# Kernel tuning notes

Measured on AMD Instinct MI355X. Metric: run time of the kernel, lower is better.

The kernel has to match this reference:

```python
import jax, jax.numpy as jnp
import numpy as np

H = 50   # hidden size (hard-coded in module)
O = 10   # fc output size


def _xavier(key, shape):
    # torch nn.init.xavier_normal_: std = sqrt(2 / (fan_in + fan_out)), fan_out=shape[0], fan_in=shape[1]
    std = (2.0 / (shape[0] + shape[1])) ** 0.5
    return jax.random.normal(key, shape, dtype=jnp.float32) * std


def setup_inputs() -> dict:
    key = jax.random.key(0)
    ks = jax.random.split(key, 9)
    B, T = 4096, 512
    x = jax.random.normal(ks[0], (B, T, 1), dtype=jnp.float32)
    z = lambda n: jnp.zeros((n,), dtype=jnp.float32)
    return {
        "x": x,
        "W_ih1": _xavier(ks[1], (H, 1)),  "W_hh1": _xavier(ks[2], (H, H)),
        "b_ih1": z(H), "b_hh1": z(H),
        "W_ih2": _xavier(ks[3], (H, H)),  "W_hh2": _xavier(ks[4], (H, H)),
        "b_ih2": z(H), "b_hh2": z(H),
        "W_ih3": _xavier(ks[5], (H, H)),  "W_hh3": _xavier(ks[6], (H, H)),
        "b_ih3": z(H), "b_hh3": z(H),
        "W_fc": _xavier(ks[7], (O, H)), "b_fc": z(O),
    }


def reference(x, W_ih1, W_hh1, b_ih1, b_hh1,
              W_ih2, W_hh2, b_ih2, b_hh2,
              W_ih3, W_hh3, b_ih3, b_hh3,
              W_fc, b_fc):
    B = x.shape[0]
    h0 = jnp.zeros((B, H), dtype=x.dtype)

    def step(carry, xt):  # xt: [B, 1]
        h1, h2, h3 = carry
        h1 = jnp.tanh(xt @ W_ih1.T + b_ih1 + h1 @ W_hh1.T + b_hh1)
        h2 = jnp.tanh(h1 @ W_ih2.T + b_ih2 + h2 @ W_hh2.T + b_hh2)
        h3 = jnp.tanh(h2 @ W_ih3.T + b_ih3 + h3 @ W_hh3.T + b_hh3)
        return (h1, h2, h3), None

    xs = jnp.swapaxes(x, 0, 1)  # [T, B, 1]
    (h1, h2, h3), _ = jax.lax.scan(step, (h0, h0, h0), xs)
    return h3 @ W_fc.T + b_fc  # [B, 10]
```

## Files before the change

kernel.cpp:

```cpp
#include <hip/hip_runtime.h>

typedef __attribute__((ext_vector_type(8))) short bf16x8;
typedef __attribute__((ext_vector_type(4))) float f32x4;

#define MFMA(a, b, c) __builtin_amdgcn_mfma_f32_16x16x32_bf16((a), (b), (c), 0, 0, 0)

#define TANH_SCALE 2.8853900817779268f

__device__ __forceinline__ short f2bf(float f) {
    union { float f; unsigned u; } v; v.f = f;
    unsigned r = v.u + 0x7fffu + ((v.u >> 16) & 1u);
    return (short)(r >> 16);
}
__device__ __forceinline__ float bf2f(short h) {
    union { unsigned u; float f; } v;
    v.u = ((unsigned)(unsigned short)h) << 16;
    return v.f;
}
__device__ __forceinline__ void wsplit(float w, short& hi, short& lo) {
    hi = f2bf(w);
    lo = f2bf(w - bf2f(hi));
}
__device__ __forceinline__ float tanh_ps(float s) {
    float z = __builtin_amdgcn_exp2f(s);
    return fmaf(-2.0f, __builtin_amdgcn_rcpf(z + 1.0f), 1.0f);
}
__device__ __forceinline__ unsigned cvt_pk_bf16(float a, float b) {
    unsigned r;
    asm("v_cvt_pk_bf16_f32 %0, %1, %2" : "=v"(r) : "v"(a), "v"(b));
    return r;
}

__device__ __forceinline__ void makeA2(const float* __restrict__ W, int jrow, int kbase,
                                       bf16x8& Ahi, bf16x8& Alo) {
#pragma unroll
    for (int i = 0; i < 8; ++i) {
        int m = kbase + i;
        short h = 0, l = 0;
        if (jrow < 50 && m < 50) wsplit(W[jrow * 50 + m] * TANH_SCALE, h, l);
        Ahi[i] = h; Alo[i] = l;
    }
}

__device__ __forceinline__ int swz(int row, int byteInRow) {
    return (row << 8) + (byteInRow ^ ((row & 15) << 4));
}
__device__ __forceinline__ bf16x8 ldsO(const short* hall, int off) {
    return *(const bf16x8*)((const char*)hall + off);
}
__device__ __forceinline__ float ldsR(const short* buf, int row, int col) {
    return bf2f(*(const short*)((const char*)buf + swz(row, col << 1)));
}

__device__ __forceinline__ void storeH(short* hall, int off, float t0, float t1, float t2, float t3) {
    uint2 hv;
    hv.x = cvt_pk_bf16(t0, t1);
    hv.y = cvt_pk_bf16(t2, t3);
    *(uint2*)((char*)hall + off) = hv;
}
__device__ __forceinline__ void storeZ(short* hall, int off) {
    uint2 zz; zz.x = 0u; zz.y = 0u;
    *(uint2*)((char*)hall + off) = zz;
}

template<bool ZOUT>
__device__ __forceinline__ void phaseX(
    short* hall, int layerid,
    int i0o, int i1o, int s0o, int s1o, int woff,
    const float* xrow, int bcol,
    const f32x4& bv, const f32x4& w1f,
    const bf16x8& Ih0, const bf16x8& Ih1,
    const bf16x8& Hh0, const bf16x8& Hh1, const bf16x8& Hl0, const bf16x8& Hl1,
    const f32x4& zc)
{
    if (layerid == 0) {
        float xf = xrow[bcol];
        f32x4 c1i;
        c1i[0] = fmaf(w1f[0], xf, bv[0]);
        c1i[1] = fmaf(w1f[1], xf, bv[1]);
        c1i[2] = fmaf(w1f[2], xf, bv[2]);
        c1i[3] = fmaf(w1f[3], xf, bv[3]);
        bf16x8 s0 = ldsO(hall, s0o), s1 = ldsO(hall, s1o);
        f32x4 c0 = MFMA(Hh0, s0, c1i);
        f32x4 c1 = MFMA(Hh1, s1, zc);
        c0 = MFMA(Hl0, s0, c0);
        c1 = MFMA(Hl1, s1, c1);
        float t0 = tanh_ps(c0[0] + c1[0]);
        float t1 = tanh_ps(c0[1] + c1[1]);
        float t2 = tanh_ps(c0[2] + c1[2]);
        float t3 = tanh_ps(c0[3] + c1[3]);
        storeH(hall, woff, t0, t1, t2, t3);
    } else {
        bf16x8 i0 = ldsO(hall, i0o), i1 = ldsO(hall, i1o);
        bf16x8 s0 = ldsO(hall, s0o), s1 = ldsO(hall, s1o);
        f32x4 c0 = MFMA(Ih0, i0, bv);
        f32x4 c1 = MFMA(Ih1, i1, zc);
        c0 = MFMA(Hh0, s0, c0);
        c1 = MFMA(Hh1, s1, c1);
        c0 = MFMA(Hl0, s0, c0);
        c1 = MFMA(Hl1, s1, c1);
        if (ZOUT) {
            storeZ(hall, woff);
        } else {
            float t0 = tanh_ps(c0[0] + c1[0]);
            float t1 = tanh_ps(c0[1] + c1[1]);
            float t2 = tanh_ps(c0[2] + c1[2]);
            float t3 = tanh_ps(c0[3] + c1[3]);
            storeH(hall, woff, t0, t1, t2, t3);
        }
    }
    __syncthreads();
}

__global__ __launch_bounds__(768, 1)
void rnn3_kernel(const float* __restrict__ x,
                 const float* __restrict__ Wih1, const float* __restrict__ Whh1,
                 const float* __restrict__ bih1, const float* __restrict__ bhh1,
                 const float* __restrict__ Wih2, const float* __restrict__ Whh2,
                 const float* __restrict__ bih2, const float* __restrict__ bhh2,
                 const float* __restrict__ Wih3, const float* __restrict__ Whh3,
                 const float* __restrict__ bih3, const float* __restrict__ bhh3,
                 const float* __restrict__ Wfc,  const float* __restrict__ bfc,
                 float* __restrict__ out)
{
    __shared__ __align__(16) short hall[6][2048];
    __shared__ float xls[514 * 17 + 8];

    const int tid  = threadIdx.x;
    const int lane = tid & 63;
    const int w    = tid >> 6;
    const int stripe  = w & 3;
    const int layerid = w >> 2;
    const int g    = lane >> 4;
    const int l15  = lane & 15;
    const int jrow = (stripe << 4) | l15;
    const int bcol = l15;
    const int jout0 = (stripe << 4) + (g << 2);
    const int b0   = blockIdx.x * 16;

    { int* z = (int*)hall; for (int k = tid; k < 6144; k += 768) z[k] = 0; }

    {
        const float4* xg = (const float4*)(x + (size_t)b0 * 512);
        for (int idx = tid; idx < 2048; idx += 768) {
            float4 v = xg[idx];
            int b = idx >> 7, t0 = (idx & 127) << 2;
            xls[(t0 + 0) * 17 + b] = v.x;
            xls[(t0 + 1) * 17 + b] = v.y;
            xls[(t0 + 2) * 17 + b] = v.z;
            xls[(t0 + 3) * 17 + b] = v.w;
        }
        if (tid < 42) xls[512 * 17 + tid] = 0.0f;
    }

    const float* WI; const float* WH; const float* bi; const float* bh;
    if (layerid == 0)      { WI = Wih1; WH = Whh1; bi = bih1; bh = bhh1; }
    else if (layerid == 1) { WI = Wih2; WH = Whh2; bi = bih2; bh = bhh2; }
    else                   { WI = Wih3; WH = Whh3; bi = bih3; bh = bhh3; }

    bf16x8 zf8 = {0,0,0,0,0,0,0,0};
    bf16x8 Ih0 = zf8, Ih1 = zf8;
    bf16x8 Hh0, Hl0, Hh1, Hl1;
    makeA2(WH, jrow, (g << 3),      Hh0, Hl0);
    makeA2(WH, jrow, 32 + (g << 3), Hh1, Hl1);
    if (layerid != 0) {
        bf16x8 d0, d1;
        makeA2(WI, jrow, (g << 3),      Ih0, d0);
        makeA2(WI, jrow, 32 + (g << 3), Ih1, d1);
    }

    f32x4 bv, w1f;
#pragma unroll
    for (int r = 0; r < 4; ++r) {
        int j = jout0 + r;
        bool v = j < 50;
        bv[r]  = v ? ((bi[j] + bh[j]) * TANH_SCALE) : 0.0f;
        w1f[r] = (layerid == 0 && v) ? (Wih1[j] * TANH_SCALE) : 0.0f;
    }
    const f32x4 zc = {0.f, 0.f, 0.f, 0.f};

    const int o0 = swz(bcol, (0 << 6) + (g << 4));
    const int o1 = swz(bcol, (1 << 6) + (g << 4));
    const int wbyte = swz(bcol, jout0 << 1);
    const int inb = (layerid == 2) ? 1 : 0;
    const int stb = layerid;
    const int A_i0 = (inb * 2 + 1) * 4096 + o0, A_i1 = (inb * 2 + 1) * 4096 + o1;
    const int A_s0 = (stb * 2 + 1) * 4096 + o0, A_s1 = (stb * 2 + 1) * 4096 + o1;
    const int B_i0 = (inb * 2 + 0) * 4096 + o0, B_i1 = (inb * 2 + 0) * 4096 + o1;
    const int B_s0 = (stb * 2 + 0) * 4096 + o0, B_s1 = (stb * 2 + 0) * 4096 + o1;
    const int wofA = (layerid * 2 + 0) * 4096 + wbyte;
    const int wofB = (layerid * 2 + 1) * 4096 + wbyte;

    __syncthreads();

    phaseX<true>(&hall[0][0], layerid, A_i0, A_i1, A_s0, A_s1, wofA,
                 &xls[0], bcol, bv, w1f, Ih0, Ih1, Hh0, Hh1, Hl0, Hl1, zc);
    if (layerid == 2) {
        phaseX<true>(&hall[0][0], layerid, B_i0, B_i1, B_s0, B_s1, wofB,
                     &xls[17], bcol, bv, w1f, Ih0, Ih1, Hh0, Hh1, Hl0, Hl1, zc);
    } else {
        phaseX<false>(&hall[0][0], layerid, B_i0, B_i1, B_s0, B_s1, wofB,
                      &xls[17], bcol, bv, w1f, Ih0, Ih1, Hh0, Hh1, Hl0, Hl1, zc);
    }

    for (int i = 2; i < 512; i += 2) {
        phaseX<false>(&hall[0][0], layerid, A_i0, A_i1, A_s0, A_s1, wofA,
                      &xls[i * 17], bcol, bv, w1f, Ih0, Ih1, Hh0, Hh1, Hl0, Hl1, zc);
        phaseX<false>(&hall[0][0], layerid, B_i0, B_i1, B_s0, B_s1, wofB,
                      &xls[(i + 1) * 17], bcol, bv, w1f, Ih0, Ih1, Hh0, Hh1, Hl0, Hl1, zc);
    }

    phaseX<false>(&hall[0][0], layerid, A_i0, A_i1, A_s0, A_s1, wofA,
                  &xls[512 * 17], bcol, bv, w1f, Ih0, Ih1, Hh0, Hh1, Hl0, Hl1, zc);
    phaseX<false>(&hall[0][0], layerid, B_i0, B_i1, B_s0, B_s1, wofB,
                  &xls[513 * 17], bcol, bv, w1f, Ih0, Ih1, Hh0, Hh1, Hl0, Hl1, zc);

    if (w < 4) {
        const short* h3f = &hall[5][0];
        int o = (w << 2) | g;
        int b = bcol;
        if (o < 10) {
            float acc = bfc[o];
            for (int k = 0; k < 50; ++k)
                acc += ldsR(h3f, b, k) * Wfc[o * 50 + k];
            out[(size_t)(b0 + b) * 10 + o] = acc;
        }
    }
}

extern "C" void kernel_launch(void* const* d_in, const int* in_sizes, int n_in,
                              void* d_out, int out_size, void* d_ws, size_t ws_size,
                              hipStream_t stream) {
    const float* x    = (const float*)d_in[0];
    const float* Wih1 = (const float*)d_in[1];
    const float* Whh1 = (const float*)d_in[2];
    const float* bih1 = (const float*)d_in[3];
    const float* bhh1 = (const float*)d_in[4];
    const float* Wih2 = (const float*)d_in[5];
    const float* Whh2 = (const float*)d_in[6];
    const float* bih2 = (const float*)d_in[7];
    const float* bhh2 = (const float*)d_in[8];
    const float* Wih3 = (const float*)d_in[9];
    const float* Whh3 = (const float*)d_in[10];
    const float* bih3 = (const float*)d_in[11];
    const float* bhh3 = (const float*)d_in[12];
    const float* Wfc  = (const float*)d_in[13];
    const float* bfc  = (const float*)d_in[14];
    float* out = (float*)d_out;

    dim3 grid(256), block(768);
    hipLaunchKernelGGL(rnn3_kernel, grid, block, 0, stream,
                       x, Wih1, Whh1, bih1, bhh1,
                       Wih2, Whh2, bih2, bhh2,
                       Wih3, Whh3, bih3, bhh3,
                       Wfc, bfc, out);
}
```

Baseline: 185.2 us.

## Merge layers 2 and 3 into one wave group, cut block to 512 threads

Restructures the wavefront-to-layer mapping so that 4 waves handle layer 1 and 4 waves compute both layers 2 and 3 together, with interleaved MFMA chains. The block shrinks from 768 to 512 threads, so fewer waves take part in each per-step barrier. The aim is to balance work, since layer 1 has fewer MFMAs, and to overlap the two independent MFMA chains inside one wave. The trade-off is that the merged waves hold twice as many weight registers and do twice the MFMA and tanh work per step, which lengthens the critical path per phase.

```diff
diff --git a/kernel.cpp b/kernel.cpp
--- a/kernel.cpp
+++ b/kernel.cpp
@@ -63,56 +63,76 @@
     *(uint2*)((char*)hall + off) = zz;
 }
 
-template<bool ZOUT>
-__device__ __forceinline__ void phaseX(
-    short* hall, int layerid,
-    int i0o, int i1o, int s0o, int s1o, int woff,
+template<bool Z2, bool Z3>
+__device__ __forceinline__ void phaseY(
+    short* hall, bool isL1,
+    int r1a, int r1b, int r2a, int r2b, int r3a, int r3b,
+    int wo1, int wo2, int wo3,
     const float* xrow, int bcol,
-    const f32x4& bv, const f32x4& w1f,
-    const bf16x8& Ih0, const bf16x8& Ih1,
-    const bf16x8& Hh0, const bf16x8& Hh1, const bf16x8& Hl0, const bf16x8& Hl1,
+    const f32x4& b1v, const f32x4& w1f,
+    const bf16x8& A1h0, const bf16x8& A1h1, const bf16x8& A1l0, const bf16x8& A1l1,
+    const f32x4& bv2, const bf16x8& I2h0, const bf16x8& I2h1,
+    const bf16x8& H2h0, const bf16x8& H2h1, const bf16x8& H2l0, const bf16x8& H2l1,
+    const f32x4& bv3, const bf16x8& I3h0, const bf16x8& I3h1,
+    const bf16x8& H3h0, const bf16x8& H3h1, const bf16x8& H3l0, const bf16x8& H3l1,
     const f32x4& zc)
 {
-    if (layerid == 0) {
+    if (isL1) {
         float xf = xrow[bcol];
         f32x4 c1i;
-        c1i[0] = fmaf(w1f[0], xf, bv[0]);
-        c1i[1] = fmaf(w1f[1], xf, bv[1]);
-        c1i[2] = fmaf(w1f[2], xf, bv[2]);
-        c1i[3] = fmaf(w1f[3], xf, bv[3]);
-        bf16x8 s0 = ldsO(hall, s0o), s1 = ldsO(hall, s1o);
-        f32x4 c0 = MFMA(Hh0, s0, c1i);
-        f32x4 c1 = MFMA(Hh1, s1, zc);
-        c0 = MFMA(Hl0, s0, c0);
-        c1 = MFMA(Hl1, s1, c1);
+        c1i[0] = fmaf(w1f[0], xf, b1v[0]);
+        c1i[1] = fmaf(w1f[1], xf, b1v[1]);
+        c1i[2] = fmaf(w1f[2], xf, b1v[2]);
+        c1i[3] = fmaf(w1f[3], xf, b1v[3]);
+        bf16x8 s0 = ldsO(hall, r1a), s1 = ldsO(hall, r1b);
+        f32x4 c0 = MFMA(A1h0, s0, c1i);
+        f32x4 c1 = MFMA(A1h1, s1, zc);
+        c0 = MFMA(A1l0, s0, c0);
+        c1 = MFMA(A1l1, s1, c1);
         float t0 = tanh_ps(c0[0] + c1[0]);
         float t1 = tanh_ps(c0[1] + c1[1]);
         float t2 = tanh_ps(c0[2] + c1[2]);
         float t3 = tanh_ps(c0[3] + c1[3]);
-        storeH(hall, woff, t0, t1, t2, t3);
+        storeH(hall, wo1, t0, t1, t2, t3);
     } else {
-        bf16x8 i0 = ldsO(hall, i0o), i1 = ldsO(hall, i1o);
-        bf16x8 s0 = ldsO(hall, s0o), s1 = ldsO(hall, s1o);
-        f32x4 c0 = MFMA(Ih0, i0, bv);
-        f32x4 c1 = MFMA(Ih1, i1, zc);
-        c0 = MFMA(Hh0, s0, c0);
-        c1 = MFMA(Hh1, s1, c1);
-        c0 = MFMA(Hl0, s0, c0);
-        c1 = MFMA(Hl1, s1, c1);
-        if (ZOUT) {
-            storeZ(hall, woff);
+        bf16x8 i0 = ldsO(hall, r1a), i1 = ldsO(hall, r1b);
+        bf16x8 m0 = ldsO(hall, r2a), m1 = ldsO(hall, r2b);
+        bf16x8 t0v = ldsO(hall, r3a), t1v = ldsO(hall, r3b);
+        f32x4 a0 = MFMA(I2h0, i0, bv2);
+        f32x4 b0 = MFMA(I3h0, m0, bv3);
+        f32x4 a1 = MFMA(I2h1, i1, zc);
+        f32x4 b1 = MFMA(I3h1, m1, zc);
+        a0 = MFMA(H2h0, m0, a0);
+        b0 = MFMA(H3h0, t0v, b0);
+        a1 = MFMA(H2h1, m1, a1);
+        b1 = MFMA(H3h1, t1v, b1);
+        a0 = MFMA(H2l0, m0, a0);
+        b0 = MFMA(H3l0, t0v, b0);
+        a1 = MFMA(H2l1, m1, a1);
+        b1 = MFMA(H3l1, t1v, b1);
+        if (Z2) {
+            storeZ(hall, wo2);
         } else {
-            float t0 = tanh_ps(c0[0] + c1[0]);
-            float t1 = tanh_ps(c0[1] + c1[1]);
-            float t2 = tanh_ps(c0[2] + c1[2]);
-            float t3 = tanh_ps(c0[3] + c1[3]);
-            storeH(hall, woff, t0, t1, t2, t3);
+            float t0 = tanh_ps(a0[0] + a1[0]);
+            float t1 = tanh_ps(a0[1] + a1[1]);
+            float t2 = tanh_ps(a0[2] + a1[2]);
+            float t3 = tanh_ps(a0[3] + a1[3]);
+            storeH(hall, wo2, t0, t1, t2, t3);
+        }
+        if (Z3) {
+            storeZ(hall, wo3);
+        } else {
+            float t0 = tanh_ps(b0[0] + b1[0]);
+            float t1 = tanh_ps(b0[1] + b1[1]);
+            float t2 = tanh_ps(b0[2] + b1[2]);
+            float t3 = tanh_ps(b0[3] + b1[3]);
+            storeH(hall, wo3, t0, t1, t2, t3);
         }
     }
     __syncthreads();
 }
 
-__global__ __launch_bounds__(768, 1)
+__global__ __launch_bounds__(512, 1)
 void rnn3_kernel(const float* __restrict__ x,
                  const float* __restrict__ Wih1, const float* __restrict__ Whh1,
                  const float* __restrict__ bih1, const float* __restrict__ bhh1,
@@ -129,8 +149,8 @@
     const int tid  = threadIdx.x;
     const int lane = tid & 63;
     const int w    = tid >> 6;
-    const int stripe  = w & 3;
-    const int layerid = w >> 2;
+    const int stripe = w & 3;
+    const bool isL1 = w < 4;
     const int g    = lane >> 4;
     const int l15  = lane & 15;
     const int jrow = (stripe << 4) | l15;
@@ -138,11 +158,11 @@
     const int jout0 = (stripe << 4) + (g << 2);
     const int b0   = blockIdx.x * 16;
 
-    { int* z = (int*)hall; for (int k = tid; k < 6144; k += 768) z[k] = 0; }
+    { int* z = (int*)hall; for (int k = tid; k < 6144; k += 512) z[k] = 0; }
 
     {
         const float4* xg = (const float4*)(x + (size_t)b0 * 512);
-        for (int idx = tid; idx < 2048; idx += 768) {
+        for (int idx = tid; idx < 2048; idx += 512) {
             float4 v = xg[idx];
             int b = idx >> 7, t0 = (idx & 127) << 2;
             xls[(t0 + 0) * 17 + b] = v.x;
@@ -153,67 +173,94 @@
         if (tid < 42) xls[512 * 17 + tid] = 0.0f;
     }
 
-    const float* WI; const float* WH; const float* bi; const float* bh;
-    if (layerid == 0)      { WI = Wih1; WH = Whh1; bi = bih1; bh = bhh1; }
-    else if (layerid == 1) { WI = Wih2; WH = Whh2; bi = bih2; bh = bhh2; }
-    else                   { WI = Wih3; WH = Whh3; bi = bih3; bh = bhh3; }
-
     bf16x8 zf8 = {0,0,0,0,0,0,0,0};
-    bf16x8 Ih0 = zf8, Ih1 = zf8;
-    bf16x8 Hh0, Hl0, Hh1, Hl1;
-    makeA2(WH, jrow, (g << 3),      Hh0, Hl0);
-    makeA2(WH, jrow, 32 + (g << 3), Hh1, Hl1);
-    if (layerid != 0) {
+    bf16x8 A1h0 = zf8, A1h1 = zf8, A1l0 = zf8, A1l1 = zf8;
+    bf16x8 I2h0 = zf8, I2h1 = zf8, H2h0 = zf8, H2h1 = zf8, H2l0 = zf8, H2l1 = zf8;
+    bf16x8 I3h0 = zf8, I3h1 = zf8, H3h0 = zf8, H3h1 = zf8, H3l0 = zf8, H3l1 = zf8;
+    f32x4 b1v = {0.f,0.f,0.f,0.f}, w1f = b1v, bv2 = b1v, bv3 = b1v;
+
+    if (isL1) {
+        makeA2(Whh1, jrow, (g << 3),      A1h0, A1l0);
+        makeA2(Whh1, jrow, 32 + (g << 3), A1h1, A1l1);
+#pragma unroll
+        for (int r = 0; r < 4; ++r) {
+            int j = jout0 + r;
+            bool v = j < 50;
+            b1v[r] = v ? ((bih1[j] + bhh1[j]) * TANH_SCALE) : 0.0f;
+            w1f[r] = v ? (Wih1[j] * TANH_SCALE) : 0.0f;
+        }
+    } else {
         bf16x8 d0, d1;
-        makeA2(WI, jrow, (g << 3),      Ih0, d0);
-        makeA2(WI, jrow, 32 + (g << 3), Ih1, d1);
-    }
-
-    f32x4 bv, w1f;
+        makeA2(Wih2, jrow, (g << 3),      I2h0, d0);
+        makeA2(Wih2, jrow, 32 + (g << 3), I2h1, d1);
+        makeA2(Whh2, jrow, (g << 3),      H2h0, H2l0);
+        makeA2(Whh2, jrow, 32 + (g << 3), H2h1, H2l1);
+        makeA2(Wih3, jrow, (g << 3),      I3h0, d0);
+        makeA2(Wih3, jrow, 32 + (g << 3), I3h1, d1);
+        makeA2(Whh3, jrow, (g << 3),      H3h0, H3l0);
+        makeA2(Whh3, jrow, 32 + (g << 3), H3h1, H3l1);
 #pragma unroll
-    for (int r = 0; r < 4; ++r) {
-        int j = jout0 + r;
-        bool v = j < 50;
-        bv[r]  = v ? ((bi[j] + bh[j]) * TANH_SCALE) : 0.0f;
-        w1f[r] = (layerid == 0 && v) ? (Wih1[j] * TANH_SCALE) : 0.0f;
+        for (int r = 0; r < 4; ++r) {
+            int j = jout0 + r;
+            bool v = j < 50;
+            bv2[r] = v ? ((bih2[j] + bhh2[j]) * TANH_SCALE) : 0.0f;
+            bv3[r] = v ? ((bih3[j] + bhh3[j]) * TANH_SCALE) : 0.0f;
+        }
     }
     const f32x4 zc = {0.f, 0.f, 0.f, 0.f};
 
     const int o0 = swz(bcol, (0 << 6) + (g << 4));
     const int o1 = swz(bcol, (1 << 6) + (g << 4));
     const int wbyte = swz(bcol, jout0 << 1);
-    const int inb = (layerid == 2) ? 1 : 0;
-    const int stb = layerid;
-    const int A_i0 = (inb * 2 + 1) * 4096 + o0, A_i1 = (inb * 2 + 1) * 4096 + o1;
-    const int A_s0 = (stb * 2 + 1) * 4096 + o0, A_s1 = (stb * 2 + 1) * 4096 + o1;
-    const int B_i0 = (inb * 2 + 0) * 4096 + o0, B_i1 = (inb * 2 + 0) * 4096 + o1;
-    const int B_s0 = (stb * 2 + 0) * 4096 + o0, B_s1 = (stb * 2 + 0) * 4096 + o1;
-    const int wofA = (layerid * 2 + 0) * 4096 + wbyte;
-    const int wofB = (layerid * 2 + 1) * 4096 + wbyte;
+    const int A_r1a = (0*2+1)*4096 + o0, A_r1b = (0*2+1)*4096 + o1;
+    const int A_r2a = (1*2+1)*4096 + o0, A_r2b = (1*2+1)*4096 + o1;
+    const int A_r3a = (2*2+1)*4096 + o0, A_r3b = (2*2+1)*4096 + o1;
+    const int A_w1  = (0*2+0)*4096 + wbyte;
+    const int A_w2  = (1*2+0)*4096 + wbyte;
+    const int A_w3  = (2*2+0)*4096 + wbyte;
+    const int B_r1a = (0*2+0)*4096 + o0, B_r1b = (0*2+0)*4096 + o1;
+    const int B_r2a = (1*2+0)*4096 + o0, B_r2b = (1*2+0)*4096 + o1;
+    const int B_r3a = (2*2+0)*4096 + o0, B_r3b = (2*2+0)*4096 + o1;
+    const int B_w1  = (0*2+1)*4096 + wbyte;
+    const int B_w2  = (1*2+1)*4096 + wbyte;
+    const int B_w3  = (2*2+1)*4096 + wbyte;
 
     __syncthreads();
 
-    phaseX<true>(&hall[0][0], layerid, A_i0, A_i1, A_s0, A_s1, wofA,
-                 &xls[0], bcol, bv, w1f, Ih0, Ih1, Hh0, Hh1, Hl0, Hl1, zc);
-    if (layerid == 2) {
-        phaseX<true>(&hall[0][0], layerid, B_i0, B_i1, B_s0, B_s1, wofB,
-                     &xls[17], bcol, bv, w1f, Ih0, Ih1, Hh0, Hh1, Hl0, Hl1, zc);
-    } else {
-        phaseX<false>(&hall[0][0], layerid, B_i0, B_i1, B_s0, B_s1, wofB,
-                      &xls[17], bcol, bv, w1f, Ih0, Ih1, Hh0, Hh1, Hl0, Hl1, zc);
-    }
+    phaseY<true, true>(&hall[0][0], isL1,
+                       A_r1a, A_r1b, A_r2a, A_r2b, A_r3a, A_r3b, A_w1, A_w2, A_w3,
+                       &xls[0], bcol, b1v, w1f, A1h0, A1h1, A1l0, A1l1,
+                       bv2, I2h0, I2h1, H2h0, H2h1, H2l0, H2l1,
+                       bv3, I3h0, I3h1, H3h0, H3h1, H3l0, H3l1, zc);
+    phaseY<false, true>(&hall[0][0], isL1,
+                        B_r1a, B_r1b, B_r2a, B_r2b, B_r3a, B_r3b, B_w1, B_w2, B_w3,
+                        &xls[17], bcol, b1v, w1f, A1h0, A1h1, A1l0, A1l1,
+                        bv2, I2h0, I2h1, H2h0, H2h1, H2l0, H2l1,
+                        bv3, I3h0, I3h1, H3h0, H3h1, H3l0, H3l1, zc);
 
     for (int i = 2; i < 512; i += 2) {
-        phaseX<false>(&hall[0][0], layerid, A_i0, A_i1, A_s0, A_s1, wofA,
-                      &xls[i * 17], bcol, bv, w1f, Ih0, Ih1, Hh0, Hh1, Hl0, Hl1, zc);
-        phaseX<false>(&hall[0][0], layerid, B_i0, B_i1, B_s0, B_s1, wofB,
-                      &xls[(i + 1) * 17], bcol, bv, w1f, Ih0, Ih1, Hh0, Hh1, Hl0, Hl1, zc);
-    }
-
-    phaseX<false>(&hall[0][0], layerid, A_i0, A_i1, A_s0, A_s1, wofA,
-                  &xls[512 * 17], bcol, bv, w1f, Ih0, Ih1, Hh0, Hh1, Hl0, Hl1, zc);
-    phaseX<false>(&hall[0][0], layerid, B_i0, B_i1, B_s0, B_s1, wofB,
-                  &xls[513 * 17], bcol, bv, w1f, Ih0, Ih1, Hh0, Hh1, Hl0, Hl1, zc);
+        phaseY<false, false>(&hall[0][0], isL1,
+                             A_r1a, A_r1b, A_r2a, A_r2b, A_r3a, A_r3b, A_w1, A_w2, A_w3,
+                             &xls[i * 17], bcol, b1v, w1f, A1h0, A1h1, A1l0, A1l1,
+                             bv2, I2h0, I2h1, H2h0, H2h1, H2l0, H2l1,
+                             bv3, I3h0, I3h1, H3h0, H3h1, H3l0, H3l1, zc);
+        phaseY<false, false>(&hall[0][0], isL1,
+                             B_r1a, B_r1b, B_r2a, B_r2b, B_r3a, B_r3b, B_w1, B_w2, B_w3,
+                             &xls[(i + 1) * 17], bcol, b1v, w1f, A1h0, A1h1, A1l0, A1l1,
+                             bv2, I2h0, I2h1, H2h0, H2h1, H2l0, H2l1,
+                             bv3, I3h0, I3h1, H3h0, H3h1, H3l0, H3l1, zc);
+    }
+
+    phaseY<false, false>(&hall[0][0], isL1,
+                         A_r1a, A_r1b, A_r2a, A_r2b, A_r3a, A_r3b, A_w1, A_w2, A_w3,
+                         &xls[512 * 17], bcol, b1v, w1f, A1h0, A1h1, A1l0, A1l1,
+                         bv2, I2h0, I2h1, H2h0, H2h1, H2l0, H2l1,
+                         bv3, I3h0, I3h1, H3h0, H3h1, H3l0, H3l1, zc);
+    phaseY<false, false>(&hall[0][0], isL1,
+                         B_r1a, B_r1b, B_r2a, B_r2b, B_r3a, B_r3b, B_w1, B_w2, B_w3,
+                         &xls[513 * 17], bcol, b1v, w1f, A1h0, A1h1, A1l0, A1l1,
+                         bv2, I2h0, I2h1, H2h0, H2h1, H2l0, H2l1,
+                         bv3, I3h0, I3h1, H3h0, H3h1, H3l0, H3l1, zc);
 
     if (w < 4) {
         const short* h3f = &hall[5][0];
@@ -248,7 +295,7 @@
     const float* bfc  = (const float*)d_in[14];
     float* out = (float*)d_out;
 
-    dim3 grid(256), block(768);
+    dim3 grid(256), block(512);
     hipLaunchKernelGGL(rnn3_kernel, grid, block, 0, stream,
                        x, Wih1, Whh1, bih1, bhh1,
                        Wih2, Whh2, bih2, bhh2,
```

Measured after the change: 226.7 us. 1.22x slower.

## Halve waves per block, each wave computing two interleaved row stripes

Applied to the files above, without the earlier changes.

The block shrinks from 12 waves to 6. Each wave now owns two 16-row output stripes of its layer instead of one. The MFMAs for the two stripes are interleaved, so independent accumulator chains can hide MFMA dependency latency, and each per-timestep barrier has fewer waves to synchronize. In exchange, each wave does twice the serial MFMA, tanh and store work per phase and holds twice the weight fragments in registers, which lengthens the per-step critical path.

```diff
diff --git a/kernel.cpp b/kernel.cpp
--- a/kernel.cpp
+++ b/kernel.cpp
@@ -64,55 +64,67 @@
 }
 
 template<bool ZOUT>
-__device__ __forceinline__ void phaseX(
-    short* hall, int layerid,
-    int i0o, int i1o, int s0o, int s1o, int woff,
+__device__ __forceinline__ void phaseP(
+    short* hall, int lay,
+    int rIa, int rIb, int rSa, int rSb, int woA, int woB,
     const float* xrow, int bcol,
-    const f32x4& bv, const f32x4& w1f,
-    const bf16x8& Ih0, const bf16x8& Ih1,
-    const bf16x8& Hh0, const bf16x8& Hh1, const bf16x8& Hl0, const bf16x8& Hl1,
+    const f32x4& bvA, const f32x4& bvB, const f32x4& w1fA, const f32x4& w1fB,
+    const bf16x8& AIh0, const bf16x8& AIh1,
+    const bf16x8& AHh0, const bf16x8& AHh1, const bf16x8& AHl0, const bf16x8& AHl1,
+    const bf16x8& BIh0, const bf16x8& BIh1,
+    const bf16x8& BHh0, const bf16x8& BHh1, const bf16x8& BHl0, const bf16x8& BHl1,
     const f32x4& zc)
 {
-    if (layerid == 0) {
+    if (lay == 0) {
         float xf = xrow[bcol];
-        f32x4 c1i;
-        c1i[0] = fmaf(w1f[0], xf, bv[0]);
-        c1i[1] = fmaf(w1f[1], xf, bv[1]);
-        c1i[2] = fmaf(w1f[2], xf, bv[2]);
-        c1i[3] = fmaf(w1f[3], xf, bv[3]);
-        bf16x8 s0 = ldsO(hall, s0o), s1 = ldsO(hall, s1o);
-        f32x4 c0 = MFMA(Hh0, s0, c1i);
-        f32x4 c1 = MFMA(Hh1, s1, zc);
-        c0 = MFMA(Hl0, s0, c0);
-        c1 = MFMA(Hl1, s1, c1);
-        float t0 = tanh_ps(c0[0] + c1[0]);
-        float t1 = tanh_ps(c0[1] + c1[1]);
-        float t2 = tanh_ps(c0[2] + c1[2]);
-        float t3 = tanh_ps(c0[3] + c1[3]);
-        storeH(hall, woff, t0, t1, t2, t3);
+        f32x4 cA, cB;
+#pragma unroll
+        for (int r = 0; r < 4; ++r) {
+            cA[r] = fmaf(w1fA[r], xf, bvA[r]);
+            cB[r] = fmaf(w1fB[r], xf, bvB[r]);
+        }
+        bf16x8 s0 = ldsO(hall, rSa), s1 = ldsO(hall, rSb);
+        f32x4 a0 = MFMA(AHh0, s0, cA);
+        f32x4 b0 = MFMA(BHh0, s0, cB);
+        f32x4 a1 = MFMA(AHh1, s1, zc);
+        f32x4 b1 = MFMA(BHh1, s1, zc);
+        a0 = MFMA(AHl0, s0, a0);
+        b0 = MFMA(BHl0, s0, b0);
+        a1 = MFMA(AHl1, s1, a1);
+        b1 = MFMA(BHl1, s1, b1);
+        storeH(hall, woA, tanh_ps(a0[0] + a1[0]), tanh_ps(a0[1] + a1[1]),
+                          tanh_ps(a0[2] + a1[2]), tanh_ps(a0[3] + a1[3]));
+        storeH(hall, woB, tanh_ps(b0[0] + b1[0]), tanh_ps(b0[1] + b1[1]),
+                          tanh_ps(b0[2] + b1[2]), tanh_ps(b0[3] + b1[3]));
     } else {
-        bf16x8 i0 = ldsO(hall, i0o), i1 = ldsO(hall, i1o);
-        bf16x8 s0 = ldsO(hall, s0o), s1 = ldsO(hall, s1o);
-        f32x4 c0 = MFMA(Ih0, i0, bv);
-        f32x4 c1 = MFMA(Ih1, i1, zc);
-        c0 = MFMA(Hh0, s0, c0);
-        c1 = MFMA(Hh1, s1, c1);
-        c0 = MFMA(Hl0, s0, c0);
-        c1 = MFMA(Hl1, s1, c1);
+        bf16x8 i0 = ldsO(hall, rIa), i1 = ldsO(hall, rIb);
+        bf16x8 s0 = ldsO(hall, rSa), s1 = ldsO(hall, rSb);
+        f32x4 a0 = MFMA(AIh0, i0, bvA);
+        f32x4 b0 = MFMA(BIh0, i0, bvB);
+        f32x4 a1 = MFMA(AIh1, i1, zc);
+        f32x4 b1 = MFMA(BIh1, i1, zc);
+        a0 = MFMA(AHh0, s0, a0);
+        b0 = MFMA(BHh0, s0, b0);
+        a1 = MFMA(AHh1, s1, a1);
+        b1 = MFMA(BHh1, s1, b1);
+        a0 = MFMA(AHl0, s0, a0);
+        b0 = MFMA(BHl0, s0, b0);
+        a1 = MFMA(AHl1, s1, a1);
+        b1 = MFMA(BHl1, s1, b1);
         if (ZOUT) {
-            storeZ(hall, woff);
+            storeZ(hall, woA);
+            storeZ(hall, woB);
         } else {
-            float t0 = tanh_ps(c0[0] + c1[0]);
-            float t1 = tanh_ps(c0[1] + c1[1]);
-            float t2 = tanh_ps(c0[2] + c1[2]);
-            float t3 = tanh_ps(c0[3] + c1[3]);
-            storeH(hall, woff, t0, t1, t2, t3);
+            storeH(hall, woA, tanh_ps(a0[0] + a1[0]), tanh_ps(a0[1] + a1[1]),
+                              tanh_ps(a0[2] + a1[2]), tanh_ps(a0[3] + a1[3]));
+            storeH(hall, woB, tanh_ps(b0[0] + b1[0]), tanh_ps(b0[1] + b1[1]),
+                              tanh_ps(b0[2] + b1[2]), tanh_ps(b0[3] + b1[3]));
         }
     }
     __syncthreads();
 }
 
-__global__ __launch_bounds__(768, 1)
+__global__ __launch_bounds__(384, 1)
 void rnn3_kernel(const float* __restrict__ x,
                  const float* __restrict__ Wih1, const float* __restrict__ Whh1,
                  const float* __restrict__ bih1, const float* __restrict__ bhh1,
@@ -129,20 +141,21 @@
     const int tid  = threadIdx.x;
     const int lane = tid & 63;
     const int w    = tid >> 6;
-    const int stripe  = w & 3;
-    const int layerid = w >> 2;
+    const int lay  = w >> 1;
+    const int sp   = w & 1;
     const int g    = lane >> 4;
     const int l15  = lane & 15;
-    const int jrow = (stripe << 4) | l15;
     const int bcol = l15;
-    const int jout0 = (stripe << 4) + (g << 2);
+    const int sA   = sp << 1, sB = sA | 1;
+    const int jrowA = (sA << 4) | l15, jrowB = (sB << 4) | l15;
+    const int joutA = (sA << 4) + (g << 2), joutB = (sB << 4) + (g << 2);
     const int b0   = blockIdx.x * 16;
 
-    { int* z = (int*)hall; for (int k = tid; k < 6144; k += 768) z[k] = 0; }
+    { int* z = (int*)hall; for (int k = tid; k < 6144; k += 384) z[k] = 0; }
 
     {
         const float4* xg = (const float4*)(x + (size_t)b0 * 512);
-        for (int idx = tid; idx < 2048; idx += 768) {
+        for (int idx = tid; idx < 2048; idx += 384) {
             float4 v = xg[idx];
             int b = idx >> 7, t0 = (idx & 127) << 2;
             xls[(t0 + 0) * 17 + b] = v.x;
@@ -154,66 +167,87 @@
     }
 
     const float* WI; const float* WH; const float* bi; const float* bh;
-    if (layerid == 0)      { WI = Wih1; WH = Whh1; bi = bih1; bh = bhh1; }
-    else if (layerid == 1) { WI = Wih2; WH = Whh2; bi = bih2; bh = bhh2; }
-    else                   { WI = Wih3; WH = Whh3; bi = bih3; bh = bhh3; }
+    if (lay == 0)      { WI = Wih1; WH = Whh1; bi = bih1; bh = bhh1; }
+    else if (lay == 1) { WI = Wih2; WH = Whh2; bi = bih2; bh = bhh2; }
+    else               { WI = Wih3; WH = Whh3; bi = bih3; bh = bhh3; }
 
     bf16x8 zf8 = {0,0,0,0,0,0,0,0};
-    bf16x8 Ih0 = zf8, Ih1 = zf8;
-    bf16x8 Hh0, Hl0, Hh1, Hl1;
-    makeA2(WH, jrow, (g << 3),      Hh0, Hl0);
-    makeA2(WH, jrow, 32 + (g << 3), Hh1, Hl1);
-    if (layerid != 0) {
+    bf16x8 AIh0 = zf8, AIh1 = zf8, BIh0 = zf8, BIh1 = zf8;
+    bf16x8 AHh0, AHh1, AHl0, AHl1, BHh0, BHh1, BHl0, BHl1;
+    makeA2(WH, jrowA, (g << 3),      AHh0, AHl0);
+    makeA2(WH, jrowA, 32 + (g << 3), AHh1, AHl1);
+    makeA2(WH, jrowB, (g << 3),      BHh0, BHl0);
+    makeA2(WH, jrowB, 32 + (g << 3), BHh1, BHl1);
+    if (lay != 0) {
         bf16x8 d0, d1;
-        makeA2(WI, jrow, (g << 3),      Ih0, d0);
-        makeA2(WI, jrow, 32 + (g << 3), Ih1, d1);
-    }
-
-    f32x4 bv, w1f;
+        makeA2(WI, jrowA, (g << 3),      AIh0, d0);
+        makeA2(WI, jrowA, 32 + (g << 3), AIh1, d1);
+        makeA2(WI, jrowB, (g << 3),      BIh0, d0);
+        makeA2(WI, jrowB, 32 + (g << 3), BIh1, d1);
+    }
+
+    f32x4 bvA, bvB, w1fA, w1fB;
 #pragma unroll
     for (int r = 0; r < 4; ++r) {
-        int j = jout0 + r;
-        bool v = j < 50;
-        bv[r]  = v ? ((bi[j] + bh[j]) * TANH_SCALE) : 0.0f;
-        w1f[r] = (layerid == 0 && v) ? (Wih1[j] * TANH_SCALE) : 0.0f;
+        int jA = joutA + r, jB = joutB + r;
+        bool vA = jA < 50, vB = jB < 50;
+        bvA[r]  = vA ? ((bi[jA] + bh[jA]) * TANH_SCALE) : 0.0f;
+        bvB[r]  = vB ? ((bi[jB] + bh[jB]) * TANH_SCALE) : 0.0f;
+        w1fA[r] = (lay == 0 && vA) ? (Wih1[jA] * TANH_SCALE) : 0.0f;
+        w1fB[r] = (lay == 0 && vB) ? (Wih1[jB] * TANH_SCALE) : 0.0f;
     }
     const f32x4 zc = {0.f, 0.f, 0.f, 0.f};
 
     const int o0 = swz(bcol, (0 << 6) + (g << 4));
     const int o1 = swz(bcol, (1 << 6) + (g << 4));
-    const int wbyte = swz(bcol, jout0 << 1);
-    const int inb = (layerid == 2) ? 1 : 0;
-    const int stb = layerid;
-    const int A_i0 = (inb * 2 + 1) * 4096 + o0, A_i1 = (inb * 2 + 1) * 4096 + o1;
-    const int A_s0 = (stb * 2 + 1) * 4096 + o0, A_s1 = (stb * 2 + 1) * 4096 + o1;
-    const int B_i0 = (inb * 2 + 0) * 4096 + o0, B_i1 = (inb * 2 + 0) * 4096 + o1;
-    const int B_s0 = (stb * 2 + 0) * 4096 + o0, B_s1 = (stb * 2 + 0) * 4096 + o1;
-    const int wofA = (layerid * 2 + 0) * 4096 + wbyte;
-    const int wofB = (layerid * 2 + 1) * 4096 + wbyte;
+    const int wbA = swz(bcol, joutA << 1);
+    const int wbB = swz(bcol, joutB << 1);
+    const int inb = (lay == 2) ? 1 : 0;
+    const int stb = lay;
+    const int A_Ia = (inb * 2 + 1) * 4096 + o0, A_Ib = (inb * 2 + 1) * 4096 + o1;
+    const int A_Sa = (stb * 2 + 1) * 4096 + o0, A_Sb = (stb * 2 + 1) * 4096 + o1;
+    const int B_Ia = (inb * 2 + 0) * 4096 + o0, B_Ib = (inb * 2 + 0) * 4096 + o1;
+    const int B_Sa = (stb * 2 + 0) * 4096 + o0, B_Sb = (stb * 2 + 0) * 4096 + o1;
+    const int A_wA = (lay * 2 + 0) * 4096 + wbA, A_wB = (lay * 2 + 0) * 4096 + wbB;
+    const int B_wA = (lay * 2 + 1) * 4096 + wbA, B_wB = (lay * 2 + 1) * 4096 + wbB;
 
     __syncthreads();
 
-    phaseX<true>(&hall[0][0], layerid, A_i0, A_i1, A_s0, A_s1, wofA,
-                 &xls[0], bcol, bv, w1f, Ih0, Ih1, Hh0, Hh1, Hl0, Hl1, zc);
-    if (layerid == 2) {
-        phaseX<true>(&hall[0][0], layerid, B_i0, B_i1, B_s0, B_s1, wofB,
-                     &xls[17], bcol, bv, w1f, Ih0, Ih1, Hh0, Hh1, Hl0, Hl1, zc);
+    phaseP<true>(&hall[0][0], lay, A_Ia, A_Ib, A_Sa, A_Sb, A_wA, A_wB,
+                 &xls[0], bcol, bvA, bvB, w1fA, w1fB,
+                 AIh0, AIh1, AHh0, AHh1, AHl0, AHl1,
+                 BIh0, BIh1, BHh0, BHh1, BHl0, BHl1, zc);
+    if (lay == 2) {
+        phaseP<true>(&hall[0][0], lay, B_Ia, B_Ib, B_Sa, B_Sb, B_wA, B_wB,
+                     &xls[17], bcol, bvA, bvB, w1fA, w1fB,
+                     AIh0, AIh1, AHh0, AHh1, AHl0, AHl1,
+                     BIh0, BIh1, BHh0, BHh1, BHl0, BHl1, zc);
     } else {
-        phaseX<false>(&hall[0][0], layerid, B_i0, B_i1, B_s0, B_s1, wofB,
-                      &xls[17], bcol, bv, w1f, Ih0, Ih1, Hh0, Hh1, Hl0, Hl1, zc);
+        phaseP<false>(&hall[0][0], lay, B_Ia, B_Ib, B_Sa, B_Sb, B_wA, B_wB,
+                      &xls[17], bcol, bvA, bvB, w1fA, w1fB,
+                      AIh0, AIh1, AHh0, AHh1, AHl0, AHl1,
+                      BIh0, BIh1, BHh0, BHh1, BHl0, BHl1, zc);
     }
 
     for (int i = 2; i < 512; i += 2) {
-        phaseX<false>(&hall[0][0], layerid, A_i0, A_i1, A_s0, A_s1, wofA,
-                      &xls[i * 17], bcol, bv, w1f, Ih0, Ih1, Hh0, Hh1, Hl0, Hl1, zc);
-        phaseX<false>(&hall[0][0], layerid, B_i0, B_i1, B_s0, B_s1, wofB,
-                      &xls[(i + 1) * 17], bcol, bv, w1f, Ih0, Ih1, Hh0, Hh1, Hl0, Hl1, zc);
-    }
-
-    phaseX<false>(&hall[0][0], layerid, A_i0, A_i1, A_s0, A_s1, wofA,
-                  &xls[512 * 17], bcol, bv, w1f, Ih0, Ih1, Hh0, Hh1, Hl0, Hl1, zc);
-    phaseX<false>(&hall[0][0], layerid, B_i0, B_i1, B_s0, B_s1, wofB,
-                  &xls[513 * 17], bcol, bv, w1f, Ih0, Ih1, Hh0, Hh1, Hl0, Hl1, zc);
+        phaseP<false>(&hall[0][0], lay, A_Ia, A_Ib, A_Sa, A_Sb, A_wA, A_wB,
+                      &xls[i * 17], bcol, bvA, bvB, w1fA, w1fB,
+                      AIh0, AIh1, AHh0, AHh1, AHl0, AHl1,
+                      BIh0, BIh1, BHh0, BHh1, BHl0, BHl1, zc);
+        phaseP<false>(&hall[0][0], lay, B_Ia, B_Ib, B_Sa, B_Sb, B_wA, B_wB,
+                      &xls[(i + 1) * 17], bcol, bvA, bvB, w1fA, w1fB,
+                      AIh0, AIh1, AHh0, AHh1, AHl0, AHl1,
+                      BIh0, BIh1, BHh0, BHh1, BHl0, BHl1, zc);
+    }
+
+    phaseP<false>(&hall[0][0], lay, A_Ia, A_Ib, A_Sa, A_Sb, A_wA, A_wB,
+                  &xls[512 * 17], bcol, bvA, bvB, w1fA, w1fB,
+                  AIh0, AIh1, AHh0, AHh1, AHl0, AHl1,
+                  BIh0, BIh1, BHh0, BHh1, BHl0, BHl1, zc);
+    phaseP<false>(&hall[0][0], lay, B_Ia, B_Ib, B_Sa, B_Sb, B_wA, B_wB,
+                  &xls[513 * 17], bcol, bvA, bvB, w1fA, w1fB,
+                  AIh0, AIh1, AHh0, AHh1, AHl0, AHl1,
+                  BIh0, BIh1, BHh0, BHh1, BHl0, BHl1, zc);
 
     if (w < 4) {
         const short* h3f = &hall[5][0];
@@ -248,7 +282,7 @@
     const float* bfc  = (const float*)d_in[14];
     float* out = (float*)d_out;
 
-    dim3 grid(256), block(768);
+    dim3 grid(256), block(384);
     hipLaunchKernelGGL(rnn3_kernel, grid, block, 0, stream,
                        x, Wih1, Whh1, bih1, bhh1,
                        Wih2, Whh2, bih2, bhh2,
```

After: 240.7 us. 29.9% more time.

## Triple-buffer hidden states and prefetch next-layer input across the barrier

Applied to the files above, without the earlier changes.

Moves from double to triple buffering of the per-layer hidden-state slots in LDS, so each layer's input from the layer below can be loaded right after the current step's MFMAs and held in registers for the next phase. This takes the input-operand LDS reads off the critical path between barriers, leaving only the recurrent-state loads before the MFMAs. The wavefront pipeline gains an extra step of skew, which adds startup phases and uses more LDS and registers.

```diff
diff --git a/kernel.cpp b/kernel.cpp
--- a/kernel.cpp
+++ b/kernel.cpp
@@ -63,24 +63,25 @@
     *(uint2*)((char*)hall + off) = zz;
 }
 
-template<bool ZOUT>
-__device__ __forceinline__ void phaseX(
-    short* hall, int layerid,
-    int i0o, int i1o, int s0o, int s1o, int woff,
+template<bool Z2, bool Z3>
+__device__ __forceinline__ void phaseS(
+    short* hall, int lay,
+    int sa, int sb, int wo, int pa, int pb,
+    bf16x8& iR0, bf16x8& iR1,
     const float* xrow, int bcol,
     const f32x4& bv, const f32x4& w1f,
     const bf16x8& Ih0, const bf16x8& Ih1,
     const bf16x8& Hh0, const bf16x8& Hh1, const bf16x8& Hl0, const bf16x8& Hl1,
     const f32x4& zc)
 {
-    if (layerid == 0) {
+    if (lay == 0) {
         float xf = xrow[bcol];
         f32x4 c1i;
         c1i[0] = fmaf(w1f[0], xf, bv[0]);
         c1i[1] = fmaf(w1f[1], xf, bv[1]);
         c1i[2] = fmaf(w1f[2], xf, bv[2]);
         c1i[3] = fmaf(w1f[3], xf, bv[3]);
-        bf16x8 s0 = ldsO(hall, s0o), s1 = ldsO(hall, s1o);
+        bf16x8 s0 = ldsO(hall, sa), s1 = ldsO(hall, sb);
         f32x4 c0 = MFMA(Hh0, s0, c1i);
         f32x4 c1 = MFMA(Hh1, s1, zc);
         c0 = MFMA(Hl0, s0, c0);
@@ -89,24 +90,26 @@
         float t1 = tanh_ps(c0[1] + c1[1]);
         float t2 = tanh_ps(c0[2] + c1[2]);
         float t3 = tanh_ps(c0[3] + c1[3]);
-        storeH(hall, woff, t0, t1, t2, t3);
+        storeH(hall, wo, t0, t1, t2, t3);
     } else {
-        bf16x8 i0 = ldsO(hall, i0o), i1 = ldsO(hall, i1o);
-        bf16x8 s0 = ldsO(hall, s0o), s1 = ldsO(hall, s1o);
-        f32x4 c0 = MFMA(Ih0, i0, bv);
-        f32x4 c1 = MFMA(Ih1, i1, zc);
+        bf16x8 s0 = ldsO(hall, sa), s1 = ldsO(hall, sb);
+        f32x4 c0 = MFMA(Ih0, iR0, bv);
+        f32x4 c1 = MFMA(Ih1, iR1, zc);
         c0 = MFMA(Hh0, s0, c0);
         c1 = MFMA(Hh1, s1, c1);
         c0 = MFMA(Hl0, s0, c0);
         c1 = MFMA(Hl1, s1, c1);
-        if (ZOUT) {
-            storeZ(hall, woff);
+        iR0 = ldsO(hall, pa);
+        iR1 = ldsO(hall, pb);
+        bool zout = (lay == 1) ? Z2 : Z3;
+        if (zout) {
+            storeZ(hall, wo);
         } else {
             float t0 = tanh_ps(c0[0] + c1[0]);
             float t1 = tanh_ps(c0[1] + c1[1]);
             float t2 = tanh_ps(c0[2] + c1[2]);
             float t3 = tanh_ps(c0[3] + c1[3]);
-            storeH(hall, woff, t0, t1, t2, t3);
+            storeH(hall, wo, t0, t1, t2, t3);
         }
     }
     __syncthreads();
@@ -123,14 +126,14 @@
                  const float* __restrict__ Wfc,  const float* __restrict__ bfc,
                  float* __restrict__ out)
 {
-    __shared__ __align__(16) short hall[6][2048];
-    __shared__ float xls[514 * 17 + 8];
+    __shared__ __align__(16) short hall[9][2048];
+    __shared__ float xls[516 * 17 + 8];
 
     const int tid  = threadIdx.x;
     const int lane = tid & 63;
     const int w    = tid >> 6;
     const int stripe  = w & 3;
-    const int layerid = w >> 2;
+    const int lay     = w >> 2;
     const int g    = lane >> 4;
     const int l15  = lane & 15;
     const int jrow = (stripe << 4) | l15;
@@ -138,7 +141,7 @@
     const int jout0 = (stripe << 4) + (g << 2);
     const int b0   = blockIdx.x * 16;
 
-    { int* z = (int*)hall; for (int k = tid; k < 6144; k += 768) z[k] = 0; }
+    { int* z = (int*)hall; for (int k = tid; k < 9216; k += 768) z[k] = 0; }
 
     {
         const float4* xg = (const float4*)(x + (size_t)b0 * 512);
@@ -150,20 +153,20 @@
             xls[(t0 + 2) * 17 + b] = v.z;
             xls[(t0 + 3) * 17 + b] = v.w;
         }
-        if (tid < 42) xls[512 * 17 + tid] = 0.0f;
+        if (tid < 76) xls[512 * 17 + tid] = 0.0f;
     }
 
     const float* WI; const float* WH; const float* bi; const float* bh;
-    if (layerid == 0)      { WI = Wih1; WH = Whh1; bi = bih1; bh = bhh1; }
-    else if (layerid == 1) { WI = Wih2; WH = Whh2; bi = bih2; bh = bhh2; }
-    else                   { WI = Wih3; WH = Whh3; bi = bih3; bh = bhh3; }
+    if (lay == 0)      { WI = Wih1; WH = Whh1; bi = bih1; bh = bhh1; }
+    else if (lay == 1) { WI = Wih2; WH = Whh2; bi = bih2; bh = bhh2; }
+    else               { WI = Wih3; WH = Whh3; bi = bih3; bh = bhh3; }
 
     bf16x8 zf8 = {0,0,0,0,0,0,0,0};
     bf16x8 Ih0 = zf8, Ih1 = zf8;
     bf16x8 Hh0, Hl0, Hh1, Hl1;
     makeA2(WH, jrow, (g << 3),      Hh0, Hl0);
     makeA2(WH, jrow, 32 + (g << 3), Hh1, Hl1);
-    if (layerid != 0) {
+    if (lay != 0) {
         bf16x8 d0, d1;
         makeA2(WI, jrow, (g << 3),      Ih0, d0);
         makeA2(WI, jrow, 32 + (g << 3), Ih1, d1);
@@ -175,48 +178,58 @@
         int j = jout0 + r;
         bool v = j < 50;
         bv[r]  = v ? ((bi[j] + bh[j]) * TANH_SCALE) : 0.0f;
-        w1f[r] = (layerid == 0 && v) ? (Wih1[j] * TANH_SCALE) : 0.0f;
+        w1f[r] = (lay == 0 && v) ? (Wih1[j] * TANH_SCALE) : 0.0f;
     }
     const f32x4 zc = {0.f, 0.f, 0.f, 0.f};
 
     const int o0 = swz(bcol, (0 << 6) + (g << 4));
     const int o1 = swz(bcol, (1 << 6) + (g << 4));
     const int wbyte = swz(bcol, jout0 << 1);
-    const int inb = (layerid == 2) ? 1 : 0;
-    const int stb = layerid;
-    const int A_i0 = (inb * 2 + 1) * 4096 + o0, A_i1 = (inb * 2 + 1) * 4096 + o1;
-    const int A_s0 = (stb * 2 + 1) * 4096 + o0, A_s1 = (stb * 2 + 1) * 4096 + o1;
-    const int B_i0 = (inb * 2 + 0) * 4096 + o0, B_i1 = (inb * 2 + 0) * 4096 + o1;
-    const int B_s0 = (stb * 2 + 0) * 4096 + o0, B_s1 = (stb * 2 + 0) * 4096 + o1;
-    const int wofA = (layerid * 2 + 0) * 4096 + wbyte;
-    const int wofB = (layerid * 2 + 1) * 4096 + wbyte;
+    const int inb = (lay == 2) ? 1 : 0;
+    const int stb = lay;
+#define REG(buf, slot) (((buf) * 3 + (slot)) * 4096)
+    const int sa0 = REG(stb, 2) + o0, sb0 = REG(stb, 2) + o1;
+    const int sa1 = REG(stb, 0) + o0, sb1 = REG(stb, 0) + o1;
+    const int sa2 = REG(stb, 1) + o0, sb2 = REG(stb, 1) + o1;
+    const int wo0 = REG(lay, 0) + wbyte;
+    const int wo1 = REG(lay, 1) + wbyte;
+    const int wo2 = REG(lay, 2) + wbyte;
+    const int pa0 = REG(inb, 2) + o0, pb0 = REG(inb, 2) + o1;
+    const int pa1 = REG(inb, 0) + o0, pb1 = REG(inb, 0) + o1;
+    const int pa2 = REG(inb, 1) + o0, pb2 = REG(inb, 1) + o1;
+#undef REG
+
+    bf16x8 iR0 = zf8, iR1 = zf8;
 
     __syncthreads();
 
-    phaseX<true>(&hall[0][0], layerid, A_i0, A_i1, A_s0, A_s1, wofA,
-                 &xls[0], bcol, bv, w1f, Ih0, Ih1, Hh0, Hh1, Hl0, Hl1, zc);
-    if (layerid == 2) {
-        phaseX<true>(&hall[0][0], layerid, B_i0, B_i1, B_s0, B_s1, wofB,
-                     &xls[17], bcol, bv, w1f, Ih0, Ih1, Hh0, Hh1, Hl0, Hl1, zc);
-    } else {
-        phaseX<false>(&hall[0][0], layerid, B_i0, B_i1, B_s0, B_s1, wofB,
-                      &xls[17], bcol, bv, w1f, Ih0, Ih1, Hh0, Hh1, Hl0, Hl1, zc);
-    }
-
-    for (int i = 2; i < 512; i += 2) {
-        phaseX<false>(&hall[0][0], layerid, A_i0, A_i1, A_s0, A_s1, wofA,
-                      &xls[i * 17], bcol, bv, w1f, Ih0, Ih1, Hh0, Hh1, Hl0, Hl1, zc);
-        phaseX<false>(&hall[0][0], layerid, B_i0, B_i1, B_s0, B_s1, wofB,
-                      &xls[(i + 1) * 17], bcol, bv, w1f, Ih0, Ih1, Hh0, Hh1, Hl0, Hl1, zc);
-    }
-
-    phaseX<false>(&hall[0][0], layerid, A_i0, A_i1, A_s0, A_s1, wofA,
-                  &xls[512 * 17], bcol, bv, w1f, Ih0, Ih1, Hh0, Hh1, Hl0, Hl1, zc);
-    phaseX<false>(&hall[0][0], layerid, B_i0, B_i1, B_s0, B_s1, wofB,
-                  &xls[513 * 17], bcol, bv, w1f, Ih0, Ih1, Hh0, Hh1, Hl0, Hl1, zc);
+    short* H = &hall[0][0];
+    phaseS<true, true>(H, lay, sa0, sb0, wo0, pa0, pb0, iR0, iR1,
+                       &xls[0 * 17], bcol, bv, w1f, Ih0, Ih1, Hh0, Hh1, Hl0, Hl1, zc);
+    phaseS<true, true>(H, lay, sa1, sb1, wo1, pa1, pb1, iR0, iR1,
+                       &xls[1 * 17], bcol, bv, w1f, Ih0, Ih1, Hh0, Hh1, Hl0, Hl1, zc);
+    phaseS<false, true>(H, lay, sa2, sb2, wo2, pa2, pb2, iR0, iR1,
+                        &xls[2 * 17], bcol, bv, w1f, Ih0, Ih1, Hh0, Hh1, Hl0, Hl1, zc);
+    phaseS<false, true>(H, lay, sa0, sb0, wo0, pa0, pb0, iR0, iR1,
+                        &xls[3 * 17], bcol, bv, w1f, Ih0, Ih1, Hh0, Hh1, Hl0, Hl1, zc);
+    phaseS<false, false>(H, lay, sa1, sb1, wo1, pa1, pb1, iR0, iR1,
+                         &xls[4 * 17], bcol, bv, w1f, Ih0, Ih1, Hh0, Hh1, Hl0, Hl1, zc);
+    phaseS<false, false>(H, lay, sa2, sb2, wo2, pa2, pb2, iR0, iR1,
+                         &xls[5 * 17], bcol, bv, w1f, Ih0, Ih1, Hh0, Hh1, Hl0, Hl1, zc);
+
+    const float* xp = &xls[6 * 17];
+    for (int it = 0; it < 170; ++it) {
+        phaseS<false, false>(H, lay, sa0, sb0, wo0, pa0, pb0, iR0, iR1,
+                             xp, bcol, bv, w1f, Ih0, Ih1, Hh0, Hh1, Hl0, Hl1, zc);
+        phaseS<false, false>(H, lay, sa1, sb1, wo1, pa1, pb1, iR0, iR1,
+                             xp + 17, bcol, bv, w1f, Ih0, Ih1, Hh0, Hh1, Hl0, Hl1, zc);
+        phaseS<false, false>(H, lay, sa2, sb2, wo2, pa2, pb2, iR0, iR1,
+                             xp + 34, bcol, bv, w1f, Ih0, Ih1, Hh0, Hh1, Hl0, Hl1, zc);
+        xp += 51;
+    }
 
     if (w < 4) {
-        const short* h3f = &hall[5][0];
+        const short* h3f = &hall[8][0];
         int o = (w << 2) | g;
         int b = bcol;
         if (o < 10) {
```

Measured after the change: 188.3 us. Within noise of the previous version (+1.7%).
